# Kernel tuning notes

Hardware: AMD Instinct MI355X
Metric: run time of the kernel (lower is better)

Reference implementation:

```python
import jax, jax.numpy as jnp
import numpy as np

B, S, H = 1, 2048, 4096
N_HEADS, N_KV, HEAD_DIM = 32, 8, 128
ROPE_THETA = 10000.0


def setup_inputs() -> dict:
    key = jax.random.key(0)
    k1, k2, k3 = jax.random.split(key, 3)
    hidden_states = jax.random.normal(k1, (B, S, H), dtype=jnp.float32)
    # fused QKV projection weight: rows = (n_heads + 2*n_kv_heads) * head_dim
    Wqkv = jax.random.normal(k2, ((N_HEADS + 2 * N_KV) * HEAD_DIM, H), dtype=jnp.float32) * 0.02
    Wo = jax.random.normal(k3, (H, N_HEADS * HEAD_DIM), dtype=jnp.float32) * 0.02
    return {"hidden_states": hidden_states, "Wqkv": Wqkv, "Wo": Wo}


def _rope_tables(seqlen, dim, theta):
    inv_freq = 1.0 / (theta ** (jnp.arange(0, dim, 2, dtype=jnp.float32) / dim))  # [dim/2]
    t = jnp.arange(seqlen, dtype=jnp.float32)
    freqs = jnp.outer(t, inv_freq)  # [S, dim/2]
    return jnp.cos(freqs), jnp.sin(freqs)


def _apply_rope(x, cos, sin):
    # torch code: reshape(...,2,-1).transpose -> view_as_complex pairs (x[j], x[j+d/2])
    # i.e. NeoX rotate-half on first/second halves of head_dim.
    d2 = x.shape[-1] // 2
    x1, x2 = x[..., :d2], x[..., d2:]
    c = cos[None, :, None, :]  # [1,S,1,d/2]
    s = sin[None, :, None, :]
    return jnp.concatenate([x1 * c - x2 * s, x1 * s + x2 * c], axis=-1)


def reference(hidden_states, Wqkv, Wo):
    b, s, h = hidden_states.shape
    # fused QKV projection
    qkv = jnp.einsum('bsh,oh->bso', hidden_states, Wqkv)
    q_end = N_HEADS * HEAD_DIM
    k_end = q_end + N_KV * HEAD_DIM
    xq = qkv[..., :q_end].reshape(b, s, N_HEADS, HEAD_DIM)
    xk = qkv[..., q_end:k_end].reshape(b, s, N_KV, HEAD_DIM)
    xv = qkv[..., k_end:].reshape(b, s, N_KV, HEAD_DIM)
    # RoPE (start_pos = 0 prefill)
    cos, sin = _rope_tables(s, HEAD_DIM, ROPE_THETA)
    xq = _apply_rope(xq, cos, sin)
    xk = _apply_rope(xk, cos, sin)
    # GQA: expand kv heads to query heads (head h uses kv head h // groups)
    groups = N_HEADS // N_KV
    xk = jnp.repeat(xk, groups, axis=2)  # [b,s,nH,hd]
    xv = jnp.repeat(xv, groups, axis=2)
    # causal attention, softmax scale 1/sqrt(head_dim) (flash_attn default, softcap=0)
    scale = 1.0 / jnp.sqrt(jnp.float32(HEAD_DIM))
    scores = jnp.einsum('bqhd,bkhd->bhqk', xq, xk) * scale
    causal = jnp.tril(jnp.ones((s, s), dtype=bool))
    scores = jnp.where(causal[None, None, :, :], scores, jnp.float32(-1e30))
    probs = jax.nn.softmax(scores, axis=-1)
    out = jnp.einsum('bhqk,bkhd->bqhd', probs, xv).reshape(b, s, N_HEADS * HEAD_DIM)
    attn_output = jnp.einsum('bsd,hd->bsh', out, Wo)
    return attn_output
```

## Files before the change

kernel.cpp:

```cpp
#include <hip/hip_runtime.h>
#include <stdint.h>

typedef unsigned short u16;
typedef unsigned int   u32;
typedef short bf16x8 __attribute__((ext_vector_type(8)));
typedef float f32x4  __attribute__((ext_vector_type(4)));

__device__ __forceinline__ u16 f2bf(float f) {
    union { float f; u32 u; } v; v.f = f;
    u32 u = v.u;
    u32 r = (u + 0x7fffu + ((u >> 16) & 1u)) >> 16;
    return (u16)r;
}
__device__ __forceinline__ float bf2f(u16 h) {
    union { u32 u; float f; } v; v.u = ((u32)h) << 16;
    return v.f;
}

__device__ __forceinline__ void gload_lds16(const void* g, void* l) {
    __builtin_amdgcn_global_load_lds(
        (__attribute__((address_space(1))) void*)g,
        (__attribute__((address_space(3))) void*)l,
        16, 0, 0);
}

__global__ __launch_bounds__(256) void cvt_all(const float4* __restrict__ s1, uint2* __restrict__ d1,
                                               const float4* __restrict__ s2, uint2* __restrict__ d2,
                                               const float4* __restrict__ s3, uint2* __restrict__ d3) {
    const float4* s; uint2* d; int i;
    int b = blockIdx.x;
    if (b < 8192)        { s = s1; d = d1; i = b * 256 + threadIdx.x; }
    else if (b < 32768)  { s = s2; d = d2; i = (b - 8192) * 256 + threadIdx.x; }
    else                 { s = s3; d = d3; i = (b - 32768) * 256 + threadIdx.x; }
    float4 v = s[i];
    uint2 o;
    o.x = (u32)f2bf(v.x) | ((u32)f2bf(v.y) << 16);
    o.y = (u32)f2bf(v.z) | ((u32)f2bf(v.w) << 16);
    d[i] = o;
}

template <typename OUT_T>
__global__ __launch_bounds__(256) void gemm_bt(const u16* __restrict__ A,
                                               const u16* __restrict__ B,
                                               OUT_T* __restrict__ C,
                                               int M, int N, int K) {
    __shared__ u16 As[2][128 * 32];
    __shared__ u16 Bs[2][128 * 32];

    const int tid  = threadIdx.x;
    const int lane = tid & 63;
    const int wv   = tid >> 6;
    const int row0 = blockIdx.y * 128;
    const int col0 = blockIdx.x * 128;

    const int wm = (wv >> 1) * 64;
    const int wn = (wv & 1) * 64;
    const int fr = lane & 15;
    const int fq = (lane >> 4) * 8;

    const int srow = lane >> 2;
    const int scol = (lane & 3) * 8;

    f32x4 acc[4][4];
#pragma unroll
    for (int i = 0; i < 4; ++i)
#pragma unroll
        for (int j = 0; j < 4; ++j) acc[i][j] = f32x4{0.f, 0.f, 0.f, 0.f};

    auto stage = [&](int buf, int k0) {
#pragma unroll
        for (int i = 0; i < 2; ++i) {
            const int chunk = wv * 2 + i;
            const int r     = chunk * 16 + srow;
            gload_lds16(A + (size_t)(row0 + r) * K + k0 + scol, &As[buf][r * 32 + scol]);
            gload_lds16(B + (size_t)(col0 + r) * K + k0 + scol, &Bs[buf][r * 32 + scol]);
        }
    };

    const int nk = K >> 5;
    stage(0, 0);

    for (int ki = 0; ki < nk; ++ki) {
        __syncthreads();
        if (ki + 1 < nk) stage((ki + 1) & 1, (ki + 1) << 5);

        const u16* as = As[ki & 1];
        const u16* bs = Bs[ki & 1];
        bf16x8 af[4], bf[4];
#pragma unroll
        for (int mt = 0; mt < 4; ++mt)
            af[mt] = *(const bf16x8*)&as[(wm + mt * 16 + fr) * 32 + fq];
#pragma unroll
        for (int nt = 0; nt < 4; ++nt)
            bf[nt] = *(const bf16x8*)&bs[(wn + nt * 16 + fr) * 32 + fq];
#pragma unroll
        for (int mt = 0; mt < 4; ++mt)
#pragma unroll
            for (int nt = 0; nt < 4; ++nt)
                acc[mt][nt] = __builtin_amdgcn_mfma_f32_16x16x32_bf16(
                    af[mt], bf[nt], acc[mt][nt], 0, 0, 0);
    }

    const int orow4 = (lane >> 4) * 4;
    const int ocol  = lane & 15;
#pragma unroll
    for (int mt = 0; mt < 4; ++mt)
#pragma unroll
        for (int nt = 0; nt < 4; ++nt)
#pragma unroll
            for (int r = 0; r < 4; ++r) {
                int mm = row0 + wm + mt * 16 + orow4 + r;
                int nn = col0 + wn + nt * 16 + ocol;
                float v = acc[mt][nt][r];
                if constexpr (sizeof(OUT_T) == 2)
                    C[(size_t)mm * N + nn] = (OUT_T)f2bf(v);
                else
                    C[(size_t)mm * N + nn] = (OUT_T)v;
            }
}

__global__ __launch_bounds__(256) void prep_kv(const u16* __restrict__ qkv,
                                               u16* __restrict__ Kb,
                                               u16* __restrict__ Vt) {
    if (blockIdx.x < 4096) {
        int id = blockIdx.x * 256 + threadIdx.x;
        int d  = id & 63;
        int t  = id >> 6;
        int kh = t & 7;
        int s  = t >> 3;
        const size_t rowbase = (size_t)s * 6144 + 4096;
        float inv = __expf(-(float)d * (9.210340371976184f / 64.0f));
        float ang = (float)s * inv;
        float cs, sn; __sincosf(ang, &sn, &cs);
        float x1 = bf2f(qkv[rowbase + kh * 128 + d]);
        float x2 = bf2f(qkv[rowbase + kh * 128 + d + 64]);
        size_t o = ((size_t)kh * 2048 + s) * 128 + d;
        Kb[o]      = f2bf(x1 * cs - x2 * sn);
        Kb[o + 64] = f2bf(x1 * sn + x2 * cs);
    } else {
        int id = (blockIdx.x - 4096) * 256 + threadIdx.x;
        int s8 = id & 255;
        int d  = (id >> 8) & 127;
        int vh = id >> 15;
        u16 tmp[8];
#pragma unroll
        for (int j = 0; j < 8; ++j)
            tmp[j] = qkv[(size_t)(s8 * 8 + j) * 6144 + 5120 + vh * 128 + d];
        *(uint4*)(Vt + ((size_t)vh * 128 + d) * 2048 + s8 * 8) = *(uint4*)tmp;
    }
}

__device__ __forceinline__ void softmax_pack(f32x4 s[4], bool diag, int w, int m, int quad,
                                             float sl2e, float& lsum, bf16x8 af[2]) {
#pragma unroll
    for (int nt = 0; nt < 4; ++nt)
#pragma unroll
        for (int r = 0; r < 4; ++r) {
            float p = __builtin_amdgcn_exp2f(s[nt][r] * sl2e);
            if (diag && (nt * 16 + quad * 4 + r > w * 16 + m)) p = 0.f;
            s[nt][r] = p;
            lsum += p;
        }
#pragma unroll
    for (int kk2 = 0; kk2 < 2; ++kk2)
#pragma unroll
        for (int ws = 0; ws < 2; ++ws) {
            u32 a, b;
            asm("v_cvt_pk_bf16_f32 %0, %1, %2"
                : "=v"(a) : "v"(s[2 * kk2][2 * ws]), "v"(s[2 * kk2][2 * ws + 1]));
            asm("v_cvt_pk_bf16_f32 %0, %1, %2"
                : "=v"(b) : "v"(s[2 * kk2 + 1][2 * ws]), "v"(s[2 * kk2 + 1][2 * ws + 1]));
            asm("v_permlane32_swap_b32 %0, %1" : "+v"(a), "+v"(b));
            asm("v_permlane16_swap_b32 %0, %1" : "+v"(a), "+v"(b));
            ((u32*)&af[kk2])[ws]     = a;
            ((u32*)&af[kk2])[ws + 2] = b;
        }
}

template <bool TWO>
__device__ __forceinline__ void attn_pass2(const bf16x8 qfA[4], const bf16x8 qfB[4],
                                           f32x4 accA[8], f32x4 accB[8],
                                           float& lA, float& lB,
                                           const u16* Ks, const u16* Vs,
                                           int w, int m, int quad,
                                           bool diagA, bool diagB, float sl2e) {
    f32x4 sA[4], sB[4];
#pragma unroll
    for (int nt = 0; nt < 4; ++nt) {
        sA[nt] = f32x4{0.f, 0.f, 0.f, 0.f};
        sB[nt] = f32x4{0.f, 0.f, 0.f, 0.f};
    }

    __builtin_amdgcn_s_setprio(1);
#pragma unroll
    for (int kk = 0; kk < 4; ++kk)
#pragma unroll
        for (int nt = 0; nt < 4; ++nt) {
            int pos = (kk * 4 + quad) ^ (m & 7);
            bf16x8 b = *(const bf16x8*)&Ks[(nt * 16 + m) * 128 + pos * 8];
            sB[nt] = __builtin_amdgcn_mfma_f32_16x16x32_bf16(b, qfB[kk], sB[nt], 0, 0, 0);
            if constexpr (TWO)
                sA[nt] = __builtin_amdgcn_mfma_f32_16x16x32_bf16(b, qfA[kk], sA[nt], 0, 0, 0);
        }
    __builtin_amdgcn_s_setprio(0);

    bf16x8 afA[2], afB[2];
    softmax_pack(sB, diagB, w, m, quad, sl2e, lB, afB);
    if constexpr (TWO) softmax_pack(sA, diagA, w, m, quad, sl2e, lA, afA);

    __builtin_amdgcn_s_setprio(1);
#pragma unroll
    for (int kk2 = 0; kk2 < 2; ++kk2)
#pragma unroll
        for (int nt = 0; nt < 8; ++nt) {
            int pos = (kk2 * 4 + quad) ^ (m & 7);
            bf16x8 b = *(const bf16x8*)&Vs[(nt * 16 + m) * 64 + pos * 8];
            accB[nt] = __builtin_amdgcn_mfma_f32_16x16x32_bf16(afB[kk2], b, accB[nt], 0, 0, 0);
            if constexpr (TWO)
                accA[nt] = __builtin_amdgcn_mfma_f32_16x16x32_bf16(afA[kk2], b, accA[nt], 0, 0, 0);
        }
    __builtin_amdgcn_s_setprio(0);
}

__global__ __launch_bounds__(256, 2) void attn_mfma(const u16* __restrict__ qkv,
                                                    const u16* __restrict__ Kb,
                                                    const u16* __restrict__ Vt,
                                                    u16* __restrict__ ctx) {
    __shared__ u16 Ks[2][64 * 128];
    __shared__ u16 Vs[2][128 * 64];

    const int tid  = threadIdx.x;
    const int lane = tid & 63;
    const int w    = tid >> 6;
    const int m    = lane & 15;
    const int quad = lane >> 4;
    const int h    = blockIdx.y;
    const int kh   = h >> 2;
    const int qtA  = blockIdx.x;
    const int qtB  = 31 - qtA;

    const u16* Ktile0 = Kb + (size_t)kh * 2048 * 128;
    const u16* Vtile0 = Vt + (size_t)kh * 128 * 2048;
    const float sl2e = 0.08838834764831845f * 1.4426950408889634f;

    auto stage = [&](int buf, int kt) {
        const u16* Kt = Ktile0 + (size_t)kt * 64 * 128;
#pragma unroll
        for (int i = 0; i < 4; ++i) {
            int slot = i * 256 + tid;
            int row = slot >> 4, cp = slot & 15;
            int gc = cp ^ (row & 7);
            gload_lds16(Kt + row * 128 + gc * 8, &Ks[buf][slot * 8]);
        }
        const u16* Vtt = Vtile0 + kt * 64;
#pragma unroll
        for (int i = 0; i < 4; ++i) {
            int slot = i * 256 + tid;
            int row = slot >> 3, cp = slot & 7;
            int gc = cp ^ (row & 7);
            gload_lds16(Vtt + (size_t)row * 2048 + gc * 8, &Vs[buf][slot * 8]);
        }
    };

    bf16x8 qa[4], qb[4];
#pragma unroll
    for (int which = 0; which < 2; ++which) {
        const int qt = which ? qtB : qtA;
        const int s  = qt * 64 + w * 16 + m;
        bf16x8 raw[4];
        const u16* qp = qkv + (size_t)s * 6144 + h * 128 + quad * 8;
#pragma unroll
        for (int kk = 0; kk < 4; ++kk)
            raw[kk] = *(const bf16x8*)(qp + kk * 32);
        bf16x8* dst = which ? qb : qa;
#pragma unroll
        for (int half = 0; half < 2; ++half)
#pragma unroll
            for (int j = 0; j < 8; ++j) {
                int d = half * 32 + quad * 8 + j;
                float inv = __expf(-(float)d * (9.210340371976184f / 64.0f));
                float ang = (float)s * inv;
                float cs, sn; __sincosf(ang, &sn, &cs);
                float x1 = bf2f(((const u16*)&raw[half])[j]);
                float x2 = bf2f(((const u16*)&raw[half + 2])[j]);
                ((u16*)&dst[half])[j]     = f2bf(x1 * cs - x2 * sn);
                ((u16*)&dst[half + 2])[j] = f2bf(x1 * sn + x2 * cs);
            }
    }

    f32x4 accA[8], accB[8];
#pragma unroll
    for (int i = 0; i < 8; ++i) { accA[i] = f32x4{0.f, 0.f, 0.f, 0.f}; accB[i] = f32x4{0.f, 0.f, 0.f, 0.f}; }
    float lA = 0.f, lB = 0.f;

    stage(0, 0);
    for (int kt = 0; kt <= qtB; ++kt) {
        __syncthreads();
        if (kt < qtB) stage((kt + 1) & 1, kt + 1);

        const u16* ks = Ks[kt & 1];
        const u16* vs = Vs[kt & 1];
        if (kt <= qtA)
            attn_pass2<true >(qa, qb, accA, accB, lA, lB, ks, vs, w, m, quad,
                              kt == qtA, false, sl2e);
        else
            attn_pass2<false>(qa, qb, accA, accB, lA, lB, ks, vs, w, m, quad,
                              false, kt == qtB, sl2e);
    }

#pragma unroll
    for (int which = 0; which < 2; ++which) {
        const int qt  = which ? qtB : qtA;
        f32x4*   acc  = which ? accB : accA;
        float    l    = which ? lB   : lA;
        l += __shfl_xor(l, 16);
        l += __shfl_xor(l, 32);
        float linv[4];
#pragma unroll
        for (int r = 0; r < 4; ++r)
            linv[r] = 1.f / __shfl(l, quad * 4 + r);
#pragma unroll
        for (int r = 0; r < 4; ++r) {
            size_t rowg = (size_t)(qt * 64 + w * 16 + quad * 4 + r);
#pragma unroll
            for (int nt = 0; nt < 8; ++nt)
                ctx[rowg * 4096 + h * 128 + nt * 16 + m] = f2bf(acc[nt][r] * linv[r]);
        }
    }
}

extern "C" void kernel_launch(void* const* d_in, const int* in_sizes, int n_in,
                              void* d_out, int out_size, void* d_ws, size_t ws_size,
                              hipStream_t stream) {
    const float* hs   = (const float*)d_in[0];
    const float* wqkv = (const float*)d_in[1];
    const float* wo   = (const float*)d_in[2];
    float* out = (float*)d_out;

    char* ws = (char*)d_ws;
    u16* hA  = (u16*)ws;  ws += (size_t)2048 * 4096 * 2;
    u16* wQ  = (u16*)ws;  ws += (size_t)6144 * 4096 * 2;
    u16* wO  = (u16*)ws;  ws += (size_t)4096 * 4096 * 2;
    u16* qkv = (u16*)ws;  ws += (size_t)2048 * 6144 * 2;
    u16* Kb  = (u16*)ws;  ws += (size_t)8 * 2048 * 128 * 2;
    u16* Vt  = (u16*)ws;  ws += (size_t)8 * 128 * 2048 * 2;
    u16* ctx = (u16*)ws;  ws += (size_t)2048 * 4096 * 2;

    cvt_all<<<49152, 256, 0, stream>>>((const float4*)hs,   (uint2*)hA,
                                       (const float4*)wqkv, (uint2*)wQ,
                                       (const float4*)wo,   (uint2*)wO);

    gemm_bt<u16><<<dim3(48, 16), 256, 0, stream>>>(hA, wQ, qkv, 2048, 6144, 4096);

    prep_kv<<<5120, 256, 0, stream>>>(qkv, Kb, Vt);

    attn_mfma<<<dim3(16, 32), 256, 0, stream>>>(qkv, Kb, Vt, ctx);

    gemm_bt<float><<<dim3(32, 16), 256, 0, stream>>>(ctx, wO, out, 2048, 4096, 4096);
}
```

Measured before the change: 505.6 us.

## Replace GEMM with 256x256-tile 8-wave kernel using swizzled LDS and phased prefetch

The 128x128, 4-wave GEMM with K=32 stages is replaced by a 256x256-tile, 512-thread kernel. It uses K=64 stages in XOR-swizzled LDS and splits each K-step into eight quadrant phases. Each phase issues part of the next tile's global-to-LDS loads while running MFMAs, using explicit waitcnt, barriers and setprio. The aim is more data reuse per tile, fewer LDS bank conflicts and better overlap of loads with compute. The trade-off is a much smaller grid (192 and 128 blocks), which may leave many CUs idle, especially for the output projection, plus large LDS use per block.

```diff
diff --git a/kernel.cpp b/kernel.cpp
--- a/kernel.cpp
+++ b/kernel.cpp
@@ -5,6 +5,8 @@
 typedef unsigned int   u32;
 typedef short bf16x8 __attribute__((ext_vector_type(8)));
 typedef float f32x4  __attribute__((ext_vector_type(4)));
+
+template <int N> struct IC { static constexpr int value = N; };
 
 __device__ __forceinline__ u16 f2bf(float f) {
     union { float f; u32 u; } v; v.f = f;
@@ -40,83 +42,138 @@
 }
 
 template <typename OUT_T>
-__global__ __launch_bounds__(256) void gemm_bt(const u16* __restrict__ A,
-                                               const u16* __restrict__ B,
-                                               OUT_T* __restrict__ C,
-                                               int M, int N, int K) {
-    __shared__ u16 As[2][128 * 32];
-    __shared__ u16 Bs[2][128 * 32];
+__global__ __launch_bounds__(512, 2) void gemm_bt8(const u16* __restrict__ A,
+                                                   const u16* __restrict__ B,
+                                                   OUT_T* __restrict__ C,
+                                                   int M, int N, int K) {
+    __shared__ u16 As[2][256 * 64];
+    __shared__ u16 Bs[2][256 * 64];
 
     const int tid  = threadIdx.x;
     const int lane = tid & 63;
     const int wv   = tid >> 6;
-    const int row0 = blockIdx.y * 128;
-    const int col0 = blockIdx.x * 128;
-
-    const int wm = (wv >> 1) * 64;
-    const int wn = (wv & 1) * 64;
+    const int row0 = blockIdx.y * 256;
+    const int col0 = blockIdx.x * 256;
+
     const int fr = lane & 15;
-    const int fq = (lane >> 4) * 8;
-
-    const int srow = lane >> 2;
-    const int scol = (lane & 3) * 8;
-
-    f32x4 acc[4][4];
-#pragma unroll
-    for (int i = 0; i < 4; ++i)
-#pragma unroll
-        for (int j = 0; j < 4; ++j) acc[i][j] = f32x4{0.f, 0.f, 0.f, 0.f};
-
-    auto stage = [&](int buf, int k0) {
-#pragma unroll
-        for (int i = 0; i < 2; ++i) {
-            const int chunk = wv * 2 + i;
-            const int r     = chunk * 16 + srow;
-            gload_lds16(A + (size_t)(row0 + r) * K + k0 + scol, &As[buf][r * 32 + scol]);
-            gload_lds16(B + (size_t)(col0 + r) * K + k0 + scol, &Bs[buf][r * 32 + scol]);
+    const int fq = lane >> 4;
+    const int u0 = (fq ^ (fr & 7)) * 8;
+    const int u1 = u0 ^ 32;
+
+    const int sr  = tid >> 3;
+    const int scp = tid & 7;
+    const int sgc = scp ^ (sr & 7);
+
+    const int wrr = (wv >> 2) * 64;
+    const int wcc = (wv & 3) * 32;
+
+    f32x4 acc[2][2][4][2];
+#pragma unroll
+    for (int a = 0; a < 2; ++a)
+#pragma unroll
+        for (int b = 0; b < 2; ++b)
+#pragma unroll
+            for (int c = 0; c < 4; ++c)
+#pragma unroll
+                for (int d = 0; d < 2; ++d) acc[a][b][c][d] = f32x4{0.f, 0.f, 0.f, 0.f};
+
+    auto stageA = [&](int buf, int half, int kt) {
+#pragma unroll
+        for (int j = 0; j < 2; ++j) {
+            int r = j * 64 + sr;
+            gload_lds16(A + (size_t)(row0 + half * 128 + r) * K + kt * 64 + sgc * 8,
+                        &As[buf][(half * 128 + r) * 64 + scp * 8]);
         }
     };
-
-    const int nk = K >> 5;
-    stage(0, 0);
-
-    for (int ki = 0; ki < nk; ++ki) {
-        __syncthreads();
-        if (ki + 1 < nk) stage((ki + 1) & 1, (ki + 1) << 5);
-
-        const u16* as = As[ki & 1];
-        const u16* bs = Bs[ki & 1];
-        bf16x8 af[4], bf[4];
-#pragma unroll
-        for (int mt = 0; mt < 4; ++mt)
-            af[mt] = *(const bf16x8*)&as[(wm + mt * 16 + fr) * 32 + fq];
-#pragma unroll
-        for (int nt = 0; nt < 4; ++nt)
-            bf[nt] = *(const bf16x8*)&bs[(wn + nt * 16 + fr) * 32 + fq];
-#pragma unroll
-        for (int mt = 0; mt < 4; ++mt)
-#pragma unroll
-            for (int nt = 0; nt < 4; ++nt)
-                acc[mt][nt] = __builtin_amdgcn_mfma_f32_16x16x32_bf16(
-                    af[mt], bf[nt], acc[mt][nt], 0, 0, 0);
-    }
-
-    const int orow4 = (lane >> 4) * 4;
-    const int ocol  = lane & 15;
-#pragma unroll
-    for (int mt = 0; mt < 4; ++mt)
-#pragma unroll
-        for (int nt = 0; nt < 4; ++nt)
-#pragma unroll
-            for (int r = 0; r < 4; ++r) {
-                int mm = row0 + wm + mt * 16 + orow4 + r;
-                int nn = col0 + wn + nt * 16 + ocol;
-                float v = acc[mt][nt][r];
-                if constexpr (sizeof(OUT_T) == 2)
-                    C[(size_t)mm * N + nn] = (OUT_T)f2bf(v);
-                else
-                    C[(size_t)mm * N + nn] = (OUT_T)v;
+    auto stageB = [&](int buf, int half, int kt) {
+#pragma unroll
+        for (int j = 0; j < 2; ++j) {
+            int r = j * 64 + sr;
+            gload_lds16(B + (size_t)(col0 + half * 128 + r) * K + kt * 64 + sgc * 8,
+                        &Bs[buf][(half * 128 + r) * 64 + scp * 8]);
+        }
+    };
+
+    auto phase = [&](auto BUFc, auto MQc, auto NQc, int vmEnd, auto&& stg) {
+        constexpr int BUF = decltype(BUFc)::value;
+        constexpr int MQ  = decltype(MQc)::value;
+        constexpr int NQ  = decltype(NQc)::value;
+        const u16* as_ = &As[BUF][(MQ * 128 + wrr + fr) * 64];
+        const u16* bs_ = &Bs[BUF][(NQ * 128 + wcc + fr) * 64];
+        bf16x8 af[4][2], bfv[2][2];
+#pragma unroll
+        for (int im = 0; im < 4; ++im) {
+            af[im][0] = *(const bf16x8*)&as_[im * 1024 + u0];
+            af[im][1] = *(const bf16x8*)&as_[im * 1024 + u1];
+        }
+#pragma unroll
+        for (int in = 0; in < 2; ++in) {
+            bfv[in][0] = *(const bf16x8*)&bs_[in * 1024 + u0];
+            bfv[in][1] = *(const bf16x8*)&bs_[in * 1024 + u1];
+        }
+        stg();
+        __builtin_amdgcn_s_barrier();
+        asm volatile("s_waitcnt lgkmcnt(0)" ::: "memory");
+        __builtin_amdgcn_sched_barrier(0);
+        __builtin_amdgcn_s_setprio(1);
+#pragma unroll
+        for (int im = 0; im < 4; ++im)
+#pragma unroll
+            for (int in = 0; in < 2; ++in) {
+                acc[MQ][NQ][im][in] = __builtin_amdgcn_mfma_f32_16x16x32_bf16(
+                    af[im][0], bfv[in][0], acc[MQ][NQ][im][in], 0, 0, 0);
+                acc[MQ][NQ][im][in] = __builtin_amdgcn_mfma_f32_16x16x32_bf16(
+                    af[im][1], bfv[in][1], acc[MQ][NQ][im][in], 0, 0, 0);
             }
+        __builtin_amdgcn_s_setprio(0);
+        if (vmEnd == 4)      asm volatile("s_waitcnt vmcnt(4)" ::: "memory");
+        else if (vmEnd == 0) asm volatile("s_waitcnt vmcnt(0)" ::: "memory");
+        __builtin_amdgcn_s_barrier();
+    };
+
+    const int nkt = K >> 6;
+    const int nit = nkt >> 1;
+
+    stageA(0, 0, 0); stageB(0, 0, 0); stageA(0, 1, 0); stageB(0, 1, 0);
+    stageA(1, 0, 1); stageB(1, 0, 1);
+    asm volatile("s_waitcnt vmcnt(4)" ::: "memory");
+    __builtin_amdgcn_s_barrier();
+
+    for (int it = 0; it < nit; ++it) {
+        const int t1 = 2 * it + 1;
+        const int t2 = 2 * it + 2;
+        const int t3 = t2 + 1;
+        const bool h2 = t2 < nkt, h3 = t3 < nkt;
+        phase(IC<0>{}, IC<0>{}, IC<0>{}, -1,          [&] { stageA(1, 1, t1); });
+        phase(IC<0>{}, IC<0>{}, IC<1>{}, -1,          [&] { stageB(1, 1, t1); });
+        phase(IC<0>{}, IC<1>{}, IC<0>{}, -1,          [&] { if (h2) stageA(0, 0, t2); });
+        phase(IC<0>{}, IC<1>{}, IC<1>{}, h2 ? 4 : 0,  [&] { if (h2) stageB(0, 0, t2); });
+        phase(IC<1>{}, IC<0>{}, IC<0>{}, -1,          [&] { if (h2) stageA(0, 1, t2); });
+        phase(IC<1>{}, IC<0>{}, IC<1>{}, -1,          [&] { if (h2) stageB(0, 1, t2); });
+        phase(IC<1>{}, IC<1>{}, IC<0>{}, -1,          [&] { if (h3) stageA(1, 0, t3); });
+        phase(IC<1>{}, IC<1>{}, IC<1>{}, 4,           [&] { if (h3) stageB(1, 0, t3); });
+    }
+
+    const int orow = (lane >> 4) * 4;
+    const int ocol = lane & 15;
+#pragma unroll
+    for (int mq = 0; mq < 2; ++mq)
+#pragma unroll
+        for (int nq = 0; nq < 2; ++nq)
+#pragma unroll
+            for (int im = 0; im < 4; ++im)
+#pragma unroll
+                for (int in = 0; in < 2; ++in)
+#pragma unroll
+                    for (int r = 0; r < 4; ++r) {
+                        int mm = row0 + mq * 128 + wrr + im * 16 + orow + r;
+                        int nn = col0 + nq * 128 + wcc + in * 16 + ocol;
+                        float v = acc[mq][nq][im][in][r];
+                        if constexpr (sizeof(OUT_T) == 2)
+                            C[(size_t)mm * N + nn] = (OUT_T)f2bf(v);
+                        else
+                            C[(size_t)mm * N + nn] = (OUT_T)v;
+                    }
 }
 
 __global__ __launch_bounds__(256) void prep_kv(const u16* __restrict__ qkv,
@@ -350,11 +407,11 @@
                                        (const float4*)wqkv, (uint2*)wQ,
                                        (const float4*)wo,   (uint2*)wO);
 
-    gemm_bt<u16><<<dim3(48, 16), 256, 0, stream>>>(hA, wQ, qkv, 2048, 6144, 4096);
+    gemm_bt8<u16><<<dim3(24, 8), 512, 0, stream>>>(hA, wQ, qkv, 2048, 6144, 4096);
 
     prep_kv<<<5120, 256, 0, stream>>>(qkv, Kb, Vt);
 
     attn_mfma<<<dim3(16, 32), 256, 0, stream>>>(qkv, Kb, Vt, ctx);
 
-    gemm_bt<float><<<dim3(32, 16), 256, 0, stream>>>(ctx, wO, out, 2048, 4096, 4096);
-}
+    gemm_bt8<float><<<dim3(16, 8), 512, 0, stream>>>(ctx, wO, out, 2048, 4096, 4096);
+}
```

Result: slower. 598.1 us (+18.3%).

## Single-buffer K tile in LDS to fit three blocks per CU

Applied to the files above, without the earlier changes.

The K tile drops from a double buffer to a single LDS buffer. The next K tile is now loaded in the middle of each iteration, after a barrier placed right after the QK^T MFMAs. V keeps its double buffer. The LDS saved, together with launch bounds raised to 3 blocks per SM, aims to raise occupancy, at the cost of an extra barrier per iteration and less lead time for the K prefetch. Correctness relies on the global_load_lds writes completing before the next iteration's barrier.

```diff
diff --git a/kernel.cpp b/kernel.cpp
--- a/kernel.cpp
+++ b/kernel.cpp
@@ -177,13 +177,14 @@
         }
 }
 
-template <bool TWO>
+template <bool TWO, typename STGK>
 __device__ __forceinline__ void attn_pass2(const bf16x8 qfA[4], const bf16x8 qfB[4],
                                            f32x4 accA[8], f32x4 accB[8],
                                            float& lA, float& lB,
                                            const u16* Ks, const u16* Vs,
                                            int w, int m, int quad,
-                                           bool diagA, bool diagB, float sl2e) {
+                                           bool diagA, bool diagB, float sl2e,
+                                           STGK&& stgK) {
     f32x4 sA[4], sB[4];
 #pragma unroll
     for (int nt = 0; nt < 4; ++nt) {
@@ -204,6 +205,9 @@
         }
     __builtin_amdgcn_s_setprio(0);
 
+    __syncthreads();
+    stgK();
+
     bf16x8 afA[2], afB[2];
     softmax_pack(sB, diagB, w, m, quad, sl2e, lB, afB);
     if constexpr (TWO) softmax_pack(sA, diagA, w, m, quad, sl2e, lA, afA);
@@ -222,11 +226,11 @@
     __builtin_amdgcn_s_setprio(0);
 }
 
-__global__ __launch_bounds__(256, 2) void attn_mfma(const u16* __restrict__ qkv,
+__global__ __launch_bounds__(256, 3) void attn_mfma(const u16* __restrict__ qkv,
                                                     const u16* __restrict__ Kb,
                                                     const u16* __restrict__ Vt,
                                                     u16* __restrict__ ctx) {
-    __shared__ u16 Ks[2][64 * 128];
+    __shared__ u16 Ks[64 * 128];
     __shared__ u16 Vs[2][128 * 64];
 
     const int tid  = threadIdx.x;
@@ -243,15 +247,17 @@
     const u16* Vtile0 = Vt + (size_t)kh * 128 * 2048;
     const float sl2e = 0.08838834764831845f * 1.4426950408889634f;
 
-    auto stage = [&](int buf, int kt) {
+    auto stageK = [&](int kt) {
         const u16* Kt = Ktile0 + (size_t)kt * 64 * 128;
 #pragma unroll
         for (int i = 0; i < 4; ++i) {
             int slot = i * 256 + tid;
             int row = slot >> 4, cp = slot & 15;
             int gc = cp ^ (row & 7);
-            gload_lds16(Kt + row * 128 + gc * 8, &Ks[buf][slot * 8]);
-        }
+            gload_lds16(Kt + row * 128 + gc * 8, &Ks[slot * 8]);
+        }
+    };
+    auto stageV = [&](int buf, int kt) {
         const u16* Vtt = Vtile0 + kt * 64;
 #pragma unroll
         for (int i = 0; i < 4; ++i) {
@@ -293,19 +299,21 @@
     for (int i = 0; i < 8; ++i) { accA[i] = f32x4{0.f, 0.f, 0.f, 0.f}; accB[i] = f32x4{0.f, 0.f, 0.f, 0.f}; }
     float lA = 0.f, lB = 0.f;
 
-    stage(0, 0);
+    stageK(0);
+    stageV(0, 0);
     for (int kt = 0; kt <= qtB; ++kt) {
         __syncthreads();
-        if (kt < qtB) stage((kt + 1) & 1, kt + 1);
-
-        const u16* ks = Ks[kt & 1];
+        if (kt < qtB) stageV((kt + 1) & 1, kt + 1);
+
         const u16* vs = Vs[kt & 1];
+        const bool last = (kt == qtB);
+        auto stgK = [&] { if (!last) stageK(kt + 1); };
         if (kt <= qtA)
-            attn_pass2<true >(qa, qb, accA, accB, lA, lB, ks, vs, w, m, quad,
-                              kt == qtA, false, sl2e);
+            attn_pass2<true >(qa, qb, accA, accB, lA, lB, Ks, vs, w, m, quad,
+                              kt == qtA, false, sl2e, stgK);
         else
-            attn_pass2<false>(qa, qb, accA, accB, lA, lB, ks, vs, w, m, quad,
-                              false, kt == qtB, sl2e);
+            attn_pass2<false>(qa, qb, accA, accB, lA, lB, Ks, vs, w, m, quad,
+                              false, kt == qtB, sl2e, stgK);
     }
 
 #pragma unroll
```

Result: slower. 654.9 us (+29.5%).
